# Performance work log

Measured on AMD Instinct MI355X. Metric: run time of the kernel, lower is better.

## Reference

```python
import jax, jax.numpy as jnp
import numpy as np

C = 64
EPS_LN = 1e-5
EPS_BN = 1e-5


def _conv1x1(x, w, b):
    # x: (B,C,H,W), w: (O,I), b: (O,)
    return jnp.einsum('oi,bihw->bohw', w, x) + b[None, :, None, None]


def _cross_attn(x_a, x_b, wq, bq, wk, bk, wv, bv):
    # query from x_a, key/value from x_b; residual onto x_a
    b, c, h, w = x_a.shape
    hw = h * w
    scale = 1.0 / jnp.sqrt(jnp.asarray(C, x_a.dtype))
    q = _conv1x1(x_a, wq, bq).reshape(b, -1, hw)   # (B,C,HW)
    k = _conv1x1(x_b, wk, bk).reshape(b, -1, hw)   # (B,C,HW)
    v = _conv1x1(x_b, wv, bv).reshape(b, -1, hw)   # (B,C,HW)
    # torch: bmm(k^T, q) -> (B,HW,HW), softmax over last dim
    logits = jnp.einsum('bci,bcj->bij', k, q) * scale
    attn = jax.nn.softmax(logits, axis=-1)
    out = jnp.einsum('bci,bij->bcj', v, attn).reshape(b, -1, h, w)
    return out + x_a


def _layernorm_ch(x, g, b):
    # LayerNorm over channel dim of (B,C,H,W)
    mu = jnp.mean(x, axis=1, keepdims=True)
    var = jnp.var(x, axis=1, keepdims=True)
    xn = (x - mu) * jax.lax.rsqrt(var + EPS_LN)
    return xn * g[None, :, None, None] + b[None, :, None, None]


def setup_inputs() -> dict:
    key = jax.random.key(0)
    ks = jax.random.split(key, 20)
    B, H, W = 4, 64, 64
    s = 0.05
    d = {
        'x_s2': jax.random.normal(ks[0], (B, C, H, W), jnp.float32),
        'x_dem': jax.random.normal(ks[1], (B, C, H, W), jnp.float32),
        'wq1': jax.random.normal(ks[2], (C, C), jnp.float32) * s,
        'bq1': jnp.zeros((C,), jnp.float32),
        'wk1': jax.random.normal(ks[3], (C, C), jnp.float32) * s,
        'bk1': jnp.zeros((C,), jnp.float32),
        'wv1': jax.random.normal(ks[4], (C, C), jnp.float32) * s,
        'bv1': jnp.zeros((C,), jnp.float32),
        'wq2': jax.random.normal(ks[5], (C, C), jnp.float32) * s,
        'bq2': jnp.zeros((C,), jnp.float32),
        'wk2': jax.random.normal(ks[6], (C, C), jnp.float32) * s,
        'bk2': jnp.zeros((C,), jnp.float32),
        'wv2': jax.random.normal(ks[7], (C, C), jnp.float32) * s,
        'bv2': jnp.zeros((C,), jnp.float32),
        'ln_s2_w': jnp.ones((C,), jnp.float32),
        'ln_s2_b': jnp.zeros((C,), jnp.float32),
        'ln_dem_w': jnp.ones((C,), jnp.float32),
        'ln_dem_b': jnp.zeros((C,), jnp.float32),
        'fw1': jax.random.normal(ks[8], (C, 2 * C, 3, 3), jnp.float32) * s,
        'fb1': jnp.zeros((C,), jnp.float32),
        'bn_g': jnp.ones((C,), jnp.float32),
        'bn_b': jnp.zeros((C,), jnp.float32),
        'fw2': jax.random.normal(ks[9], (C, C), jnp.float32) * s,
        'fb2': jnp.zeros((C,), jnp.float32),
    }
    return d


def reference(x_s2, x_dem, wq1, bq1, wk1, bk1, wv1, bv1,
              wq2, bq2, wk2, bk2, wv2, bv2,
              ln_s2_w, ln_s2_b, ln_dem_w, ln_dem_b,
              fw1, fb1, bn_g, bn_b, fw2, fb2):
    out_s2 = _cross_attn(x_s2, x_dem, wq1, bq1, wk1, bk1, wv1, bv1)
    out_dem = _cross_attn(x_dem, x_s2, wq2, bq2, wk2, bk2, wv2, bv2)
    out_s2 = _layernorm_ch(out_s2, ln_s2_w, ln_s2_b)
    out_dem = _layernorm_ch(out_dem, ln_dem_w, ln_dem_b)
    combined = jnp.concatenate([out_s2, out_dem], axis=1)  # (B,2C,H,W)
    y = jax.lax.conv_general_dilated(
        combined, fw1, window_strides=(1, 1), padding='SAME',
        dimension_numbers=('NCHW', 'OIHW', 'NCHW')) + fb1[None, :, None, None]
    # BatchNorm2d in training mode: batch statistics over (B,H,W)
    mu = jnp.mean(y, axis=(0, 2, 3), keepdims=True)
    var = jnp.var(y, axis=(0, 2, 3), keepdims=True)
    y = (y - mu) * jax.lax.rsqrt(var + EPS_BN)
    y = y * bn_g[None, :, None, None] + bn_b[None, :, None, None]
    y = jax.nn.relu(y)
    return _conv1x1(y, fw2, fb2)
```

## Files before the change

### kernel.cpp

```cpp
#include <hip/hip_runtime.h>
#include <hip/hip_bf16.h>


using bf16x8 = __attribute__((ext_vector_type(8))) short;
using f32x4  = __attribute__((ext_vector_type(4))) float;
using f32x16 = __attribute__((ext_vector_type(16))) float;
typedef unsigned int uint2v __attribute__((ext_vector_type(2)));

#define MFMA16(a, b, c) __builtin_amdgcn_mfma_f32_16x16x32_bf16((a), (b), (c), 0, 0, 0)
#define MFMA32(a, b, c) __builtin_amdgcn_mfma_f32_32x32x16_bf16((a), (b), (c), 0, 0, 0)

constexpr int B_ = 4, C_ = 64, S_ = 4096;
constexpr float kQS = 0.18033688f;

constexpr size_t OFF_XT   = 0;
constexpr size_t OFF_WB   = 4u * 1024 * 1024;
constexpr size_t OFF_FW1R = OFF_WB + 64 * 1024;
constexpr size_t OFF_QT   = OFF_FW1R + 160 * 1024;
constexpr size_t OFF_KT   = OFF_QT + 4u * 1024 * 1024;
constexpr size_t OFF_V    = OFF_KT + 4u * 1024 * 1024;
constexpr size_t OFF_COMB = OFF_V + 4u * 1024 * 1024;
constexpr size_t OFF_Y    = OFF_COMB + 4u * 1024 * 1024;
constexpr size_t OFF_PART = OFF_Y + 4u * 1024 * 1024;
constexpr size_t OFF_BNA  = OFF_PART + 128 * 1024;
constexpr size_t OFF_BNB  = OFF_BNA + 1024;

__device__ __forceinline__ unsigned short f2bf(float f) {
  unsigned int u = __float_as_uint(f);
  unsigned int r = (u + 0x7fffu + ((u >> 16) & 1u)) >> 16;
  return (unsigned short)r;
}
__device__ __forceinline__ unsigned int cvt_pk_bf16(float lo, float hi) {
  unsigned int r;
  asm("v_cvt_pk_bf16_f32 %0, %1, %2" : "=v"(r) : "v"(lo), "v"(hi));
  return r;
}
__device__ __forceinline__ float fast_exp2(float x) {
#if __has_builtin(__builtin_amdgcn_exp2f)
  return __builtin_amdgcn_exp2f(x);
#else
  return exp2f(x);
#endif
}
__device__ __forceinline__ void plswap(unsigned int& a, unsigned int& b) {
  uint2v r = __builtin_amdgcn_permlane32_swap(a, b, false, false);
  a = r[0];
  b = r[1];
}

__device__ __forceinline__ void build_pv_frags(const f32x16 s, float& lsum,
                                               bf16x8* out) {
  float p[16];
#pragma unroll
  for (int r = 0; r < 16; ++r) p[r] = fast_exp2(s[r]);
  lsum += (((p[0] + p[1]) + (p[2] + p[3])) + ((p[4] + p[5]) + (p[6] + p[7]))) +
          (((p[8] + p[9]) + (p[10] + p[11])) + ((p[12] + p[13]) + (p[14] + p[15])));
#pragma unroll
  for (int h = 0; h < 2; ++h) {
    unsigned int X  = cvt_pk_bf16(p[8 * h + 0], p[8 * h + 1]);
    unsigned int X2 = cvt_pk_bf16(p[8 * h + 2], p[8 * h + 3]);
    unsigned int Y  = cvt_pk_bf16(p[8 * h + 4], p[8 * h + 5]);
    unsigned int Y2 = cvt_pk_bf16(p[8 * h + 6], p[8 * h + 7]);
    plswap(X, Y);
    plswap(X2, Y2);
    union { unsigned int u[4]; bf16x8 v; } bb;
    bb.u[0] = X; bb.u[1] = X2; bb.u[2] = Y; bb.u[3] = Y2;
    out[h] = bb.v;
  }
}

__global__ void k_prep(const float* wq1, const float* wk1, const float* wv1,
                       const float* wq2, const float* wk2, const float* wv2,
                       const float* fw2, const float* fw1,
                       const float* xs2, const float* xdem,
                       unsigned short* wb, unsigned short* fw1r,
                       unsigned short* xT) {
  __shared__ float lds[64][65];
  if (blockIdx.x < 400) {
    int g = blockIdx.x * 256 + threadIdx.x;
    if (g < 7 * 4096) {
      int m = g >> 12, idx = g & 4095;
      const float* src[7] = {wq1, wk1, wv1, wq2, wk2, wv2, fw2};
      float sc = (m == 0 || m == 3) ? kQS : 1.0f;
      wb[g] = f2bf(src[m][idx] * sc);
    } else {
      int t = g - 7 * 4096;
      if (t < 64 * 1152) {
        int o = t / 1152, kk = t % 1152;
        int dydx = kk >> 7, ci = kk & 127;
        fw1r[t] = f2bf(fw1[o * 1152 + ci * 9 + dydx]);
      }
    }
    return;
  }
  int bid = blockIdx.x - 400;
  int pt = bid & 63, b = (bid >> 6) & 3, tz = bid >> 8;
  int tid = threadIdx.x;
  const float* src = (tz == 0) ? xs2 : xdem;
  int p0 = pt * 64;
#pragma unroll
  for (int k = 0; k < 16; ++k) {
    int idx = k * 256 + tid;
    int c = idx >> 6, pp = idx & 63;
    lds[c][pp] = src[((size_t)(b * 64 + c) << 12) + p0 + pp];
  }
  __syncthreads();
  unsigned short* dst = xT + (size_t)tz * (B_ * S_ * C_);
#pragma unroll
  for (int k = 0; k < 4; ++k) {
    int p = (tid >> 4) + k * 16;
    int c0 = (tid & 15) * 4;
    ushort4 v;
    v.x = f2bf(lds[c0 + 0][p]);
    v.y = f2bf(lds[c0 + 1][p]);
    v.z = f2bf(lds[c0 + 2][p]);
    v.w = f2bf(lds[c0 + 3][p]);
    *(ushort4*)&dst[((size_t)((b << 12) + p0 + p)) * 64 + c0] = v;
  }
}

__global__ __launch_bounds__(256) void k_proj(
    const unsigned short* xT, const unsigned short* wb,
    const float* bq1, const float* bk1, const float* bv1,
    const float* bq2, const float* bk2, const float* bv2,
    unsigned short* Qf, unsigned short* Kf, unsigned short* Vf) {
  int pc = blockIdx.x, b = blockIdx.y, dir = blockIdx.z;
  int lane = threadIdx.x & 63, wid = threadIdx.x >> 6;
  int l4 = lane & 15, g4 = lane >> 4;
  const unsigned short* xq =
      xT + ((size_t)(dir * B_ + b)) * (size_t)(S_ * C_);
  const unsigned short* xkv =
      xT + ((size_t)((1 - dir) * B_ + b)) * (size_t)(S_ * C_);
  size_t dbOff = ((size_t)dir * B_ + b) * (size_t)(S_ * C_);
  const float* bq = dir ? bq2 : bq1;
  const float* bk = dir ? bk2 : bk1;
  const float* bv = dir ? bv2 : bv1;
  int pbase = pc * 64 + wid * 16;

  bf16x8 aq[2], akv[2];
#pragma unroll
  for (int kc = 0; kc < 2; ++kc) {
    aq[kc] = *(const bf16x8*)&xq[(size_t)(pbase + l4) * 64 + kc * 32 + g4 * 8];
    akv[kc] = *(const bf16x8*)&xkv[(size_t)(pbase + l4) * 64 + kc * 32 + g4 * 8];
  }

#pragma unroll
  for (int prod = 0; prod < 2; ++prod) {
    const unsigned short* wm = wb + (dir * 3 + prod) * 4096;
    unsigned short* dst = (prod == 0 ? Qf : Kf) + dbOff;
    const float* bp = (prod == 0) ? bq : bk;
    float bscale = (prod == 0) ? kQS : 1.0f;
    const bf16x8* af = (prod == 0) ? aq : akv;
#pragma unroll
    for (int nt = 0; nt < 4; ++nt) {
      bf16x8 wf0 = *(const bf16x8*)&wm[(nt * 16 + l4) * 64 + g4 * 8];
      bf16x8 wf1 = *(const bf16x8*)&wm[(nt * 16 + l4) * 64 + 32 + g4 * 8];
      f32x4 acc = {0.f, 0.f, 0.f, 0.f};
      acc = MFMA16(af[0], wf0, acc);
      acc = MFMA16(af[1], wf1, acc);
      float bias_c = bp[nt * 16 + l4] * bscale;
#pragma unroll
      for (int r = 0; r < 4; ++r)
        dst[(size_t)nt * 65536 + (size_t)(pbase + g4 * 4 + r) * 16 + l4] =
            f2bf(acc[r] + bias_c);
    }
  }
  {
    const unsigned short* wm = wb + (dir * 3 + 2) * 4096;
    unsigned short* dst = Vf + dbOff;
#pragma unroll
    for (int mt = 0; mt < 4; ++mt) {
      bf16x8 wf0 = *(const bf16x8*)&wm[(mt * 16 + l4) * 64 + g4 * 8];
      bf16x8 wf1 = *(const bf16x8*)&wm[(mt * 16 + l4) * 64 + 32 + g4 * 8];
      f32x4 acc = {0.f, 0.f, 0.f, 0.f};
      acc = MFMA16(wf0, akv[0], acc);
      acc = MFMA16(wf1, akv[1], acc);
#pragma unroll
      for (int r = 0; r < 4; ++r) {
        int c = mt * 16 + g4 * 4 + r;
        dst[(size_t)(pbase >> 4) * 1024 + c * 16 + l4] = f2bf(acc[r] + bv[c]);
      }
    }
  }
}

constexpr int TST = 72;

__global__ __launch_bounds__(256, 2) void k_attn(
    const unsigned short* Qf, const unsigned short* Kf, const unsigned short* Vf,
    const float* xs2, const float* xdem,
    const float* lnw_s2, const float* lnb_s2,
    const float* lnw_dem, const float* lnb_dem,
    unsigned short* comb) {
  __shared__ __align__(16) char smem[34816];
  const f32x16 kZero16 = {0.f, 0.f, 0.f, 0.f, 0.f, 0.f, 0.f, 0.f,
                          0.f, 0.f, 0.f, 0.f, 0.f, 0.f, 0.f, 0.f};
  int bd = blockIdx.x, jb = blockIdx.y;
  int dir = bd >> 2, b = bd & 3;
  int lane = threadIdx.x & 63, wid = threadIdx.x >> 6;
  int l5 = lane & 31;
  int h = lane >> 5;
  int hi8 = h * 8, hi4 = h * 4;
  size_t dbOff = (size_t)bd * (size_t)(S_ * C_);
  const unsigned short* qp = Qf + dbOff;
  const unsigned short* kp = Kf + dbOff;
  const unsigned short* vp = Vf + dbOff;

  int jbase = jb * 64;
  bf16x8 qf[2][4];
#pragma unroll
  for (int jg = 0; jg < 2; ++jg)
#pragma unroll
    for (int kc = 0; kc < 4; ++kc)
      qf[jg][kc] = *(const bf16x8*)&qp[(size_t)kc * 65536 +
                                       (size_t)(jbase + jg * 32 + l5) * 16 + hi8];

  f32x16 acc00 = kZero16, acc01 = kZero16, acc10 = kZero16, acc11 = kZero16;
  float lsum0 = 0.f, lsum1 = 0.f;
  int ibeg = wid * 1024;

  for (int t = 0; t < 32; ++t) {
    int i0 = ibeg + t * 32;
    bf16x8 ak[4], av[4];
#pragma unroll
    for (int k = 0; k < 4; ++k)
      ak[k] = *(const bf16x8*)&kp[(size_t)k * 65536 + (size_t)(i0 + l5) * 16 + hi8];
    int ic = i0 >> 4;
    av[0] = *(const bf16x8*)&vp[(size_t)ic * 1024 + l5 * 16 + hi8];
    av[1] = *(const bf16x8*)&vp[(size_t)(ic + 1) * 1024 + l5 * 16 + hi8];
    av[2] = *(const bf16x8*)&vp[(size_t)ic * 1024 + (32 + l5) * 16 + hi8];
    av[3] = *(const bf16x8*)&vp[(size_t)(ic + 1) * 1024 + (32 + l5) * 16 + hi8];

    f32x16 S0 = kZero16;
    S0 = MFMA32(ak[0], qf[0][0], S0);
    S0 = MFMA32(ak[1], qf[0][1], S0);
    S0 = MFMA32(ak[2], qf[0][2], S0);
    S0 = MFMA32(ak[3], qf[0][3], S0);
    bf16x8 pb0[2];
    build_pv_frags(S0, lsum0, pb0);
    f32x16 S1 = kZero16;
    S1 = MFMA32(ak[0], qf[1][0], S1);
    S1 = MFMA32(ak[1], qf[1][1], S1);
    S1 = MFMA32(ak[2], qf[1][2], S1);
    S1 = MFMA32(ak[3], qf[1][3], S1);
    bf16x8 pb1[2];
    build_pv_frags(S1, lsum1, pb1);

    acc00 = MFMA32(av[0], pb0[0], acc00);
    acc00 = MFMA32(av[1], pb0[1], acc00);
    acc01 = MFMA32(av[2], pb0[0], acc01);
    acc01 = MFMA32(av[3], pb0[1], acc01);
    acc10 = MFMA32(av[0], pb1[0], acc10);
    acc10 = MFMA32(av[1], pb1[1], acc10);
    acc11 = MFMA32(av[2], pb1[0], acc11);
    acc11 = MFMA32(av[3], pb1[1], acc11);
  }

  float* Lp = (float*)(smem + 32768);
  Lp[wid * 128 + lane] = lsum0;
  Lp[wid * 128 + 64 + lane] = lsum1;

#define STORE1(A_, CIDX, RG)                                              \
  {                                                                       \
    _Pragma("unroll") for (int q2 = 0; q2 < 4; ++q2) {                    \
      f32x4 tv = {(A_)[q2 * 4 + 0], (A_)[q2 * 4 + 1],                     \
                  (A_)[q2 * 4 + 2], (A_)[q2 * 4 + 3]};                    \
      *(f32x4*)&(RG)[((CIDX) * 4 + q2) * 256 + lane * 4] = tv;            \
    }                                                                     \
  }
#define ADD1(A_, CIDX, RR)                                                \
  {                                                                       \
    _Pragma("unroll") for (int q2 = 0; q2 < 4; ++q2) {                    \
      f32x4 tv = *(const f32x4*)&(RR)[((CIDX) * 4 + q2) * 256 + lane * 4];\
      _Pragma("unroll") for (int e = 0; e < 4; ++e) (A_)[q2 * 4 + e] += tv[e]; \
    }                                                                     \
  }
#define PUB(SLOT)                                                         \
  {                                                                       \
    float* rg_ = (float*)(smem + (size_t)(SLOT) * 16384);                 \
    STORE1(acc00, 0, rg_) STORE1(acc01, 1, rg_)                           \
    STORE1(acc10, 2, rg_) STORE1(acc11, 3, rg_)                           \
  }
#define ADDP(SLOT)                                                        \
  {                                                                       \
    const float* rr_ = (const float*)(smem + (size_t)(SLOT) * 16384);     \
    ADD1(acc00, 0, rr_) ADD1(acc01, 1, rr_)                               \
    ADD1(acc10, 2, rr_) ADD1(acc11, 3, rr_)                               \
  }

  if (wid >= 2) PUB(wid - 2)
  __syncthreads();
  if (wid < 2) ADDP(wid)
  __syncthreads();
  if (wid == 1) PUB(0)
  __syncthreads();
  if (wid != 0) return;
  ADDP(0)
#undef PUB
#undef ADDP
#undef STORE1
#undef ADD1

  const float* xa = (dir == 0 ? xs2 : xdem) + (size_t)b * C_ * S_;
  const float* lw = (dir == 0) ? lnw_s2 : lnw_dem;
  const float* lbp = (dir == 0) ? lnb_s2 : lnb_dem;
  unsigned short* T = (unsigned short*)smem;

#pragma unroll
  for (int jg = 0; jg < 2; ++jg) {
    float ls = 0.f;
#pragma unroll
    for (int w = 0; w < 4; ++w) ls += Lp[w * 128 + jg * 64 + lane];
    ls += __shfl_xor(ls, 32);
    float linv = 1.0f / ls;
    int jcol = jbase + jg * 32 + l5;

    float vals[32];
    float s1 = 0.f, s2 = 0.f;
#pragma unroll
    for (int ct = 0; ct < 2; ++ct)
#pragma unroll
      for (int reg = 0; reg < 16; ++reg) {
        int c = ct * 32 + (reg & 3) + 8 * (reg >> 2) + hi4;
        float a_ = (jg == 0) ? (ct == 0 ? acc00[reg] : acc01[reg])
                             : (ct == 0 ? acc10[reg] : acc11[reg]);
        float v = a_ * linv + xa[(size_t)c * S_ + jcol];
        vals[ct * 16 + reg] = v;
        s1 += v;
        s2 += v * v;
      }
    s1 += __shfl_xor(s1, 32);
    s2 += __shfl_xor(s2, 32);
    float mean = s1 * (1.0f / 64.0f);
    float var = s2 * (1.0f / 64.0f) - mean * mean;
    float rstd = rsqrtf(var + 1e-5f);

#pragma unroll
    for (int ct = 0; ct < 2; ++ct)
#pragma unroll
      for (int q2 = 0; q2 < 4; ++q2)
#pragma unroll
        for (int pp = 0; pp < 2; ++pp) {
          int r0 = q2 * 4 + pp * 2;
          int c0 = ct * 32 + 8 * q2 + hi4 + pp * 2;
          float x0 = (vals[ct * 16 + r0 + 0] - mean) * rstd * lw[c0 + 0] + lbp[c0 + 0];
          float x1 = (vals[ct * 16 + r0 + 1] - mean) * rstd * lw[c0 + 1] + lbp[c0 + 1];
          *(unsigned int*)&T[l5 * TST + c0] = cvt_pk_bf16(x0, x1);
        }
    int j_l = lane >> 1, cc = (lane & 1) * 32;
    unsigned short* cb =
        comb + ((size_t)b * S_ + jbase + jg * 32 + j_l) * 128 + dir * 64 + cc;
    const unsigned short* ts = &T[j_l * TST + cc];
#pragma unroll
    for (int q = 0; q < 4; ++q) {
      uint4 tq = *(const uint4*)&ts[q * 8];
      *(uint4*)&cb[q * 8] = tq;
    }
  }
}

__global__ __launch_bounds__(256) void k_conv3(const unsigned short* comb,
                                               const unsigned short* fw1r,
                                               const float* fb1, float* y,
                                               float* part) {
  __shared__ float red[4][128];
  int pc = blockIdx.x, b = blockIdx.y;
  int lane = threadIdx.x & 63, wid = threadIdx.x >> 6;
  int l4 = lane & 15, g4 = lane >> 4;
  int p0 = pc * 64 + wid * 16;
  int p_l = p0 + l4;
  int py0 = p_l >> 6, px0 = p_l & 63;
  f32x4 acc[4];
#pragma unroll
  for (int ot = 0; ot < 4; ++ot) acc[ot] = f32x4{0.f, 0.f, 0.f, 0.f};

#pragma unroll
  for (int kk9 = 0; kk9 < 9; ++kk9) {
    int py = py0 + (kk9 / 3) - 1;
    int px = px0 + (kk9 % 3) - 1;
    bool ok = (py >= 0) && (py < 64) && (px >= 0) && (px < 64);
    const unsigned short* base = comb + ((size_t)(b << 12) + py * 64 + px) * 128;
#pragma unroll
    for (int kc = 0; kc < 4; ++kc) {
      bf16x8 af = {0, 0, 0, 0, 0, 0, 0, 0};
      if (ok) af = *(const bf16x8*)&base[kc * 32 + g4 * 8];
#pragma unroll
      for (int ot = 0; ot < 4; ++ot) {
        bf16x8 bfr = *(const bf16x8*)&fw1r[(size_t)(ot * 16 + l4) * 1152 + kk9 * 128 + kc * 32 + g4 * 8];
        acc[ot] = MFMA16(af, bfr, acc[ot]);
      }
    }
  }
  float ps[4], ps2[4];
#pragma unroll
  for (int ot = 0; ot < 4; ++ot) {
    float bias = fb1[ot * 16 + l4];
    float s = 0.f, s2 = 0.f;
#pragma unroll
    for (int r = 0; r < 4; ++r) {
      float v = acc[ot][r] + bias;
      y[((size_t)(b << 12) + p0 + g4 * 4 + r) * 64 + ot * 16 + l4] = v;
      s += v;
      s2 += v * v;
    }
    s += __shfl_xor(s, 16);
    s += __shfl_xor(s, 32);
    s2 += __shfl_xor(s2, 16);
    s2 += __shfl_xor(s2, 32);
    ps[ot] = s;
    ps2[ot] = s2;
  }
  if (lane < 16) {
#pragma unroll
    for (int ot = 0; ot < 4; ++ot) {
      red[wid][ot * 16 + lane] = ps[ot];
      red[wid][64 + ot * 16 + lane] = ps2[ot];
    }
  }
  __syncthreads();
  if (wid == 0) {
    int o = lane;
    float s = red[0][o] + red[1][o] + red[2][o] + red[3][o];
    float s2 = red[0][64 + o] + red[1][64 + o] + red[2][64 + o] + red[3][64 + o];
    int blk = b * 64 + pc;
    part[(blk * 64 + o) * 2 + 0] = s;
    part[(blk * 64 + o) * 2 + 1] = s2;
  }
}

__global__ void k_bnfin(const float* part, const float* bng, const float* bnb,
                        float* bnA, float* bnB) {
  int o = threadIdx.x;
  float s = 0.f, s2 = 0.f;
  for (int k = 0; k < 256; ++k) {
    s += part[(k * 64 + o) * 2 + 0];
    s2 += part[(k * 64 + o) * 2 + 1];
  }
  float mean = s * (1.0f / 16384.0f);
  float var = s2 * (1.0f / 16384.0f) - mean * mean;
  float a = bng[o] * rsqrtf(var + 1e-5f);
  bnA[o] = a;
  bnB[o] = bnb[o] - mean * a;
}

__global__ __launch_bounds__(128) void k_final(const float* y, const unsigned short* fw2b,
                                               const float* bnA, const float* bnB,
                                               const float* fb2, float* out) {
  int pc = blockIdx.x, b = blockIdx.y;
  int lane = threadIdx.x & 63, wid = threadIdx.x >> 6;
  int l4 = lane & 15, g4 = lane >> 4;
  int p0 = pc * 32 + wid * 16;

  bf16x8 afw[4][2];
#pragma unroll
  for (int mt = 0; mt < 4; ++mt)
#pragma unroll
    for (int kc = 0; kc < 2; ++kc)
      afw[mt][kc] = *(const bf16x8*)&fw2b[(mt * 16 + l4) * 64 + kc * 32 + g4 * 8];
  float a8[2][8], b8[2][8];
#pragma unroll
  for (int kc = 0; kc < 2; ++kc)
#pragma unroll
    for (int e = 0; e < 8; ++e) {
      int c = kc * 32 + g4 * 8 + e;
      a8[kc][e] = bnA[c];
      b8[kc][e] = bnB[c];
    }
  float fbv[4][4];
#pragma unroll
  for (int mt = 0; mt < 4; ++mt)
#pragma unroll
    for (int r = 0; r < 4; ++r) fbv[mt][r] = fb2[mt * 16 + g4 * 4 + r];

  f32x4 acc[4];
#pragma unroll
  for (int mt = 0; mt < 4; ++mt) acc[mt] = f32x4{0.f, 0.f, 0.f, 0.f};

#pragma unroll
  for (int kc = 0; kc < 2; ++kc) {
    const float* yrow = &y[((size_t)(b << 12) + p0 + l4) * 64 + kc * 32 + g4 * 8];
    float4 y0 = *(const float4*)yrow;
    float4 y1 = *(const float4*)(yrow + 4);
    float zv[8] = {y0.x, y0.y, y0.z, y0.w, y1.x, y1.y, y1.z, y1.w};
    bf16x8 zf;
#pragma unroll
    for (int e = 0; e < 8; ++e)
      zf[e] = (short)f2bf(fmaxf(zv[e] * a8[kc][e] + b8[kc][e], 0.f));
#pragma unroll
    for (int mt = 0; mt < 4; ++mt) acc[mt] = MFMA16(afw[mt][kc], zf, acc[mt]);
  }
#pragma unroll
  for (int mt = 0; mt < 4; ++mt)
#pragma unroll
    for (int r = 0; r < 4; ++r)
      out[((size_t)b * 64 + mt * 16 + g4 * 4 + r) * (size_t)S_ + p0 + l4] =
          acc[mt][r] + fbv[mt][r];
}

extern "C" void kernel_launch(void* const* d_in, const int* in_sizes, int n_in,
                              void* d_out, int out_size, void* d_ws, size_t ws_size,
                              hipStream_t stream) {
  const float* x_s2 = (const float*)d_in[0];
  const float* x_dem = (const float*)d_in[1];
  const float* wq1 = (const float*)d_in[2];
  const float* bq1 = (const float*)d_in[3];
  const float* wk1 = (const float*)d_in[4];
  const float* bk1 = (const float*)d_in[5];
  const float* wv1 = (const float*)d_in[6];
  const float* bv1 = (const float*)d_in[7];
  const float* wq2 = (const float*)d_in[8];
  const float* bq2 = (const float*)d_in[9];
  const float* wk2 = (const float*)d_in[10];
  const float* bk2 = (const float*)d_in[11];
  const float* wv2 = (const float*)d_in[12];
  const float* bv2 = (const float*)d_in[13];
  const float* ln_s2_w = (const float*)d_in[14];
  const float* ln_s2_b = (const float*)d_in[15];
  const float* ln_dem_w = (const float*)d_in[16];
  const float* ln_dem_b = (const float*)d_in[17];
  const float* fw1 = (const float*)d_in[18];
  const float* fb1 = (const float*)d_in[19];
  const float* bn_g = (const float*)d_in[20];
  const float* bn_b = (const float*)d_in[21];
  const float* fw2 = (const float*)d_in[22];
  const float* fb2 = (const float*)d_in[23];

  char* ws = (char*)d_ws;
  unsigned short* xT = (unsigned short*)(ws + OFF_XT);
  unsigned short* wbuf = (unsigned short*)(ws + OFF_WB);
  unsigned short* fw1r = (unsigned short*)(ws + OFF_FW1R);
  unsigned short* Qf = (unsigned short*)(ws + OFF_QT);
  unsigned short* Kf = (unsigned short*)(ws + OFF_KT);
  unsigned short* Vf = (unsigned short*)(ws + OFF_V);
  unsigned short* comb = (unsigned short*)(ws + OFF_COMB);
  float* ybuf = (float*)(ws + OFF_Y);
  float* part = (float*)(ws + OFF_PART);
  float* bnA = (float*)(ws + OFF_BNA);
  float* bnB = (float*)(ws + OFF_BNB);

  k_prep<<<912, 256, 0, stream>>>(wq1, wk1, wv1, wq2, wk2, wv2, fw2, fw1,
                                  x_s2, x_dem, wbuf, fw1r, xT);
  k_proj<<<dim3(64, 4, 2), 256, 0, stream>>>(xT, wbuf, bq1, bk1, bv1,
                                             bq2, bk2, bv2, Qf, Kf, Vf);
  k_attn<<<dim3(8, 64), 256, 0, stream>>>(Qf, Kf, Vf, x_s2, x_dem,
                                          ln_s2_w, ln_s2_b, ln_dem_w, ln_dem_b,
                                          comb);
  k_conv3<<<dim3(64, 4), 256, 0, stream>>>(comb, fw1r, fb1, ybuf, part);
  k_bnfin<<<1, 64, 0, stream>>>(part, bn_g, bn_b, bnA, bnB);
  k_final<<<dim3(128, 4), 128, 0, stream>>>(ybuf, wbuf + 6 * 4096, bnA, bnB, fb2,
                                            (float*)d_out);
}
```

Baseline: 100.8 us.

## Double-buffer attention K/V loads and split conv3/final output channels across more blocks

```diff
diff --git a/kernel.cpp b/kernel.cpp
--- a/kernel.cpp
+++ b/kernel.cpp
@@ -22,7 +22,7 @@
 constexpr size_t OFF_COMB = OFF_V + 4u * 1024 * 1024;
 constexpr size_t OFF_Y    = OFF_COMB + 4u * 1024 * 1024;
 constexpr size_t OFF_PART = OFF_Y + 4u * 1024 * 1024;
-constexpr size_t OFF_BNA  = OFF_PART + 128 * 1024;
+constexpr size_t OFF_BNA  = OFF_PART + 512 * 1024;
 constexpr size_t OFF_BNB  = OFF_BNA + 1024;
 
 __device__ __forceinline__ unsigned short f2bf(float f) {
@@ -219,42 +219,55 @@
   float lsum0 = 0.f, lsum1 = 0.f;
   int ibeg = wid * 1024;
 
-  for (int t = 0; t < 32; ++t) {
-    int i0 = ibeg + t * 32;
-    bf16x8 ak[4], av[4];
-#pragma unroll
-    for (int k = 0; k < 4; ++k)
-      ak[k] = *(const bf16x8*)&kp[(size_t)k * 65536 + (size_t)(i0 + l5) * 16 + hi8];
-    int ic = i0 >> 4;
-    av[0] = *(const bf16x8*)&vp[(size_t)ic * 1024 + l5 * 16 + hi8];
-    av[1] = *(const bf16x8*)&vp[(size_t)(ic + 1) * 1024 + l5 * 16 + hi8];
-    av[2] = *(const bf16x8*)&vp[(size_t)ic * 1024 + (32 + l5) * 16 + hi8];
-    av[3] = *(const bf16x8*)&vp[(size_t)(ic + 1) * 1024 + (32 + l5) * 16 + hi8];
-
-    f32x16 S0 = kZero16;
-    S0 = MFMA32(ak[0], qf[0][0], S0);
-    S0 = MFMA32(ak[1], qf[0][1], S0);
-    S0 = MFMA32(ak[2], qf[0][2], S0);
-    S0 = MFMA32(ak[3], qf[0][3], S0);
-    bf16x8 pb0[2];
-    build_pv_frags(S0, lsum0, pb0);
-    f32x16 S1 = kZero16;
-    S1 = MFMA32(ak[0], qf[1][0], S1);
-    S1 = MFMA32(ak[1], qf[1][1], S1);
-    S1 = MFMA32(ak[2], qf[1][2], S1);
-    S1 = MFMA32(ak[3], qf[1][3], S1);
-    bf16x8 pb1[2];
-    build_pv_frags(S1, lsum1, pb1);
-
-    acc00 = MFMA32(av[0], pb0[0], acc00);
-    acc00 = MFMA32(av[1], pb0[1], acc00);
-    acc01 = MFMA32(av[2], pb0[0], acc01);
-    acc01 = MFMA32(av[3], pb0[1], acc01);
-    acc10 = MFMA32(av[0], pb1[0], acc10);
-    acc10 = MFMA32(av[1], pb1[1], acc10);
-    acc11 = MFMA32(av[2], pb1[0], acc11);
-    acc11 = MFMA32(av[3], pb1[1], acc11);
-  }
+#define LOADT(AK, AV, I0)                                                    \
+  {                                                                          \
+    int i0_ = (I0);                                                          \
+    _Pragma("unroll") for (int k_ = 0; k_ < 4; ++k_)                         \
+        (AK)[k_] = *(const bf16x8*)&kp[(size_t)k_ * 65536 +                  \
+                                       (size_t)(i0_ + l5) * 16 + hi8];       \
+    int ic_ = i0_ >> 4;                                                      \
+    (AV)[0] = *(const bf16x8*)&vp[(size_t)ic_ * 1024 + l5 * 16 + hi8];       \
+    (AV)[1] = *(const bf16x8*)&vp[(size_t)(ic_ + 1) * 1024 + l5 * 16 + hi8]; \
+    (AV)[2] = *(const bf16x8*)&vp[(size_t)ic_ * 1024 + (32 + l5) * 16 + hi8];\
+    (AV)[3] = *(const bf16x8*)&vp[(size_t)(ic_ + 1) * 1024 + (32 + l5) * 16 + hi8];\
+  }
+
+#define TILE(AK, AV)                                                         \
+  {                                                                          \
+    f32x16 S0 = kZero16;                                                     \
+    S0 = MFMA32((AK)[0], qf[0][0], S0);                                      \
+    S0 = MFMA32((AK)[1], qf[0][1], S0);                                      \
+    S0 = MFMA32((AK)[2], qf[0][2], S0);                                      \
+    S0 = MFMA32((AK)[3], qf[0][3], S0);                                      \
+    bf16x8 pb0[2];                                                           \
+    build_pv_frags(S0, lsum0, pb0);                                          \
+    f32x16 S1 = kZero16;                                                     \
+    S1 = MFMA32((AK)[0], qf[1][0], S1);                                      \
+    S1 = MFMA32((AK)[1], qf[1][1], S1);                                      \
+    S1 = MFMA32((AK)[2], qf[1][2], S1);                                      \
+    S1 = MFMA32((AK)[3], qf[1][3], S1);                                      \
+    bf16x8 pb1[2];                                                           \
+    build_pv_frags(S1, lsum1, pb1);                                          \
+    acc00 = MFMA32((AV)[0], pb0[0], acc00);                                  \
+    acc00 = MFMA32((AV)[1], pb0[1], acc00);                                  \
+    acc01 = MFMA32((AV)[2], pb0[0], acc01);                                  \
+    acc01 = MFMA32((AV)[3], pb0[1], acc01);                                  \
+    acc10 = MFMA32((AV)[0], pb1[0], acc10);                                  \
+    acc10 = MFMA32((AV)[1], pb1[1], acc10);                                  \
+    acc11 = MFMA32((AV)[2], pb1[0], acc11);                                  \
+    acc11 = MFMA32((AV)[3], pb1[1], acc11);                                  \
+  }
+
+  bf16x8 akA[4], avA[4], akB[4], avB[4];
+  LOADT(akA, avA, ibeg)
+  for (int t = 0; t < 32; t += 2) {
+    LOADT(akB, avB, ibeg + ((t + 1) & 31) * 32)
+    TILE(akA, avA)
+    LOADT(akA, avA, ibeg + ((t + 2) & 31) * 32)
+    TILE(akB, avB)
+  }
+#undef LOADT
+#undef TILE
 
   float* Lp = (float*)(smem + 32768);
   Lp[wid * 128 + lane] = lsum0;
@@ -359,20 +372,19 @@
   }
 }
 
-__global__ __launch_bounds__(256) void k_conv3(const unsigned short* comb,
+__global__ __launch_bounds__(128) void k_conv3(const unsigned short* comb,
                                                const unsigned short* fw1r,
                                                const float* fb1, float* y,
                                                float* part) {
-  __shared__ float red[4][128];
   int pc = blockIdx.x, b = blockIdx.y;
   int lane = threadIdx.x & 63, wid = threadIdx.x >> 6;
   int l4 = lane & 15, g4 = lane >> 4;
-  int p0 = pc * 64 + wid * 16;
+  int p0 = pc * 16;
   int p_l = p0 + l4;
   int py0 = p_l >> 6, px0 = p_l & 63;
-  f32x4 acc[4];
-#pragma unroll
-  for (int ot = 0; ot < 4; ++ot) acc[ot] = f32x4{0.f, 0.f, 0.f, 0.f};
+  f32x4 acc[2];
+#pragma unroll
+  for (int o = 0; o < 2; ++o) acc[o] = f32x4{0.f, 0.f, 0.f, 0.f};
 
 #pragma unroll
   for (int kk9 = 0; kk9 < 9; ++kk9) {
@@ -385,20 +397,22 @@
       bf16x8 af = {0, 0, 0, 0, 0, 0, 0, 0};
       if (ok) af = *(const bf16x8*)&base[kc * 32 + g4 * 8];
 #pragma unroll
-      for (int ot = 0; ot < 4; ++ot) {
+      for (int o = 0; o < 2; ++o) {
+        int ot = wid * 2 + o;
         bf16x8 bfr = *(const bf16x8*)&fw1r[(size_t)(ot * 16 + l4) * 1152 + kk9 * 128 + kc * 32 + g4 * 8];
-        acc[ot] = MFMA16(af, bfr, acc[ot]);
+        acc[o] = MFMA16(af, bfr, acc[o]);
       }
     }
   }
-  float ps[4], ps2[4];
-#pragma unroll
-  for (int ot = 0; ot < 4; ++ot) {
+  int blk = b * 256 + pc;
+#pragma unroll
+  for (int o = 0; o < 2; ++o) {
+    int ot = wid * 2 + o;
     float bias = fb1[ot * 16 + l4];
     float s = 0.f, s2 = 0.f;
 #pragma unroll
     for (int r = 0; r < 4; ++r) {
-      float v = acc[ot][r] + bias;
+      float v = acc[o][r] + bias;
       y[((size_t)(b << 12) + p0 + g4 * 4 + r) * 64 + ot * 16 + l4] = v;
       s += v;
       s2 += v * v;
@@ -407,40 +421,35 @@
     s += __shfl_xor(s, 32);
     s2 += __shfl_xor(s2, 16);
     s2 += __shfl_xor(s2, 32);
-    ps[ot] = s;
-    ps2[ot] = s2;
-  }
-  if (lane < 16) {
-#pragma unroll
-    for (int ot = 0; ot < 4; ++ot) {
-      red[wid][ot * 16 + lane] = ps[ot];
-      red[wid][64 + ot * 16 + lane] = ps2[ot];
-    }
-  }
-  __syncthreads();
-  if (wid == 0) {
-    int o = lane;
-    float s = red[0][o] + red[1][o] + red[2][o] + red[3][o];
-    float s2 = red[0][64 + o] + red[1][64 + o] + red[2][64 + o] + red[3][64 + o];
-    int blk = b * 64 + pc;
-    part[(blk * 64 + o) * 2 + 0] = s;
-    part[(blk * 64 + o) * 2 + 1] = s2;
+    if (lane < 16) {
+      part[((size_t)blk * 64 + ot * 16 + lane) * 2 + 0] = s;
+      part[((size_t)blk * 64 + ot * 16 + lane) * 2 + 1] = s2;
+    }
   }
 }
 
 __global__ void k_bnfin(const float* part, const float* bng, const float* bnb,
                         float* bnA, float* bnB) {
-  int o = threadIdx.x;
+  __shared__ float red[2][256];
+  int t = threadIdx.x;
+  int o = t & 63, q = t >> 6;
   float s = 0.f, s2 = 0.f;
-  for (int k = 0; k < 256; ++k) {
-    s += part[(k * 64 + o) * 2 + 0];
-    s2 += part[(k * 64 + o) * 2 + 1];
-  }
-  float mean = s * (1.0f / 16384.0f);
-  float var = s2 * (1.0f / 16384.0f) - mean * mean;
-  float a = bng[o] * rsqrtf(var + 1e-5f);
-  bnA[o] = a;
-  bnB[o] = bnb[o] - mean * a;
+  for (int k = q; k < 1024; k += 4) {
+    s += part[((size_t)k * 64 + o) * 2 + 0];
+    s2 += part[((size_t)k * 64 + o) * 2 + 1];
+  }
+  red[0][t] = s;
+  red[1][t] = s2;
+  __syncthreads();
+  if (t < 64) {
+    float a = red[0][t] + red[0][t + 64] + red[0][t + 128] + red[0][t + 192];
+    float c = red[1][t] + red[1][t + 64] + red[1][t + 128] + red[1][t + 192];
+    float mean = a * (1.0f / 16384.0f);
+    float var = c * (1.0f / 16384.0f) - mean * mean;
+    float g = bng[t] * rsqrtf(var + 1e-5f);
+    bnA[t] = g;
+    bnB[t] = bnb[t] - mean * g;
+  }
 }
 
 __global__ __launch_bounds__(128) void k_final(const float* y, const unsigned short* fw2b,
@@ -449,14 +458,14 @@
   int pc = blockIdx.x, b = blockIdx.y;
   int lane = threadIdx.x & 63, wid = threadIdx.x >> 6;
   int l4 = lane & 15, g4 = lane >> 4;
-  int p0 = pc * 32 + wid * 16;
-
-  bf16x8 afw[4][2];
-#pragma unroll
-  for (int mt = 0; mt < 4; ++mt)
+  int p0 = pc * 16;
+
+  bf16x8 afw[2][2];
+#pragma unroll
+  for (int m = 0; m < 2; ++m)
 #pragma unroll
     for (int kc = 0; kc < 2; ++kc)
-      afw[mt][kc] = *(const bf16x8*)&fw2b[(mt * 16 + l4) * 64 + kc * 32 + g4 * 8];
+      afw[m][kc] = *(const bf16x8*)&fw2b[((wid * 2 + m) * 16 + l4) * 64 + kc * 32 + g4 * 8];
   float a8[2][8], b8[2][8];
 #pragma unroll
   for (int kc = 0; kc < 2; ++kc)
@@ -466,15 +475,15 @@
       a8[kc][e] = bnA[c];
       b8[kc][e] = bnB[c];
     }
-  float fbv[4][4];
-#pragma unroll
-  for (int mt = 0; mt < 4; ++mt)
-#pragma unroll
-    for (int r = 0; r < 4; ++r) fbv[mt][r] = fb2[mt * 16 + g4 * 4 + r];
-
-  f32x4 acc[4];
-#pragma unroll
-  for (int mt = 0; mt < 4; ++mt) acc[mt] = f32x4{0.f, 0.f, 0.f, 0.f};
+  float fbv[2][4];
+#pragma unroll
+  for (int m = 0; m < 2; ++m)
+#pragma unroll
+    for (int r = 0; r < 4; ++r) fbv[m][r] = fb2[(wid * 2 + m) * 16 + g4 * 4 + r];
+
+  f32x4 acc[2];
+#pragma unroll
+  for (int m = 0; m < 2; ++m) acc[m] = f32x4{0.f, 0.f, 0.f, 0.f};
 
 #pragma unroll
   for (int kc = 0; kc < 2; ++kc) {
@@ -487,14 +496,14 @@
     for (int e = 0; e < 8; ++e)
       zf[e] = (short)f2bf(fmaxf(zv[e] * a8[kc][e] + b8[kc][e], 0.f));
 #pragma unroll
-    for (int mt = 0; mt < 4; ++mt) acc[mt] = MFMA16(afw[mt][kc], zf, acc[mt]);
-  }
-#pragma unroll
-  for (int mt = 0; mt < 4; ++mt)
+    for (int m = 0; m < 2; ++m) acc[m] = MFMA16(afw[m][kc], zf, acc[m]);
+  }
+#pragma unroll
+  for (int m = 0; m < 2; ++m)
 #pragma unroll
     for (int r = 0; r < 4; ++r)
-      out[((size_t)b * 64 + mt * 16 + g4 * 4 + r) * (size_t)S_ + p0 + l4] =
-          acc[mt][r] + fbv[mt][r];
+      out[((size_t)b * 64 + (wid * 2 + m) * 16 + g4 * 4 + r) * (size_t)S_ + p0 + l4] =
+          acc[m][r] + fbv[m][r];
 }
 
 extern "C" void kernel_launch(void* const* d_in, const int* in_sizes, int n_in,
@@ -545,8 +554,8 @@
   k_attn<<<dim3(8, 64), 256, 0, stream>>>(Qf, Kf, Vf, x_s2, x_dem,
                                           ln_s2_w, ln_s2_b, ln_dem_w, ln_dem_b,
                                           comb);
-  k_conv3<<<dim3(64, 4), 256, 0, stream>>>(comb, fw1r, fb1, ybuf, part);
-  k_bnfin<<<1, 64, 0, stream>>>(part, bn_g, bn_b, bnA, bnB);
-  k_final<<<dim3(128, 4), 128, 0, stream>>>(ybuf, wbuf + 6 * 4096, bnA, bnB, fb2,
+  k_conv3<<<dim3(256, 4), 128, 0, stream>>>(comb, fw1r, fb1, ybuf, part);
+  k_bnfin<<<1, 256, 0, stream>>>(part, bn_g, bn_b, bnA, bnB);
+  k_final<<<dim3(256, 4), 128, 0, stream>>>(ybuf, wbuf + 6 * 4096, bnA, bnB, fb2,
                                             (float*)d_out);
 }
```

Measured after the change: 152.1 us. 50.9% more time.
